# Optimization experiments

Hardware: AMD Instinct MI355X
Metric: run time of the kernel (lower is better)

The kernel has to match this reference:

```python
import jax, jax.numpy as jnp
import numpy as np

N, E, F = 20000, 320000, 128
H = 2 * F  # MLP width = 256
EPS = 1e-5
TANH_ALPHA = 1.0


def setup_inputs() -> dict:
    key = jax.random.key(0)
    ks = jax.random.split(key, 16)
    x = jax.random.normal(ks[0], (N, F), dtype=jnp.float32)
    edge_index = jax.random.randint(ks[1], (2, E), 0, N, dtype=jnp.int64)
    s = 1.0 / np.sqrt(H)
    W1 = jax.random.uniform(ks[2], (H, H), jnp.float32, -s, s)
    b1 = jax.random.uniform(ks[3], (H,), jnp.float32, -s, s)
    g1 = jnp.ones((H,), jnp.float32)
    be1 = jnp.zeros((H,), jnp.float32)
    rm1 = jax.random.normal(ks[4], (H,), jnp.float32) * 0.1
    rv1 = jax.random.uniform(ks[5], (H,), jnp.float32, 0.5, 1.5)
    W2 = jax.random.uniform(ks[6], (H, H), jnp.float32, -s, s)
    b2 = jax.random.uniform(ks[7], (H,), jnp.float32, -s, s)
    g2 = jnp.ones((H,), jnp.float32)
    be2 = jnp.zeros((H,), jnp.float32)
    rm2 = jax.random.normal(ks[8], (H,), jnp.float32) * 0.1
    rv2 = jax.random.uniform(ks[9], (H,), jnp.float32, 0.5, 1.5)
    W3 = jax.random.uniform(ks[10], (F, H), jnp.float32, -s, s)
    b3 = jax.random.uniform(ks[11], (F,), jnp.float32, -s, s)
    return {"x": x, "edge_index": edge_index,
            "W1": W1, "b1": b1, "g1": g1, "be1": be1, "rm1": rm1, "rv1": rv1,
            "W2": W2, "b2": b2, "g2": g2, "be2": be2, "rm2": rm2, "rv2": rv2,
            "W3": W3, "b3": b3}


def _block(h, W, b, g, be, rm, rv):
    # Linear -> (Dropout inactive at eval) -> BatchNorm1d (eval, running stats) -> ReLU
    h = h @ W.T + b
    h = (h - rm) * (g * jax.lax.rsqrt(rv + EPS)) + be
    return jax.nn.relu(h)


def reference(x, edge_index, W1, b1, g1, be1, rm1, rv1,
              W2, b2, g2, be2, rm2, rv2, W3, b3):
    src, dst = edge_index[0], edge_index[1]  # PyG: x_j = x[src], x_i = x[dst]
    xi = x[dst]                              # [E, F]
    xj = x[src]                              # [E, F]
    h = jnp.concatenate([xi, xj - xi], axis=-1)  # [E, 2F]
    h = _block(h, W1, b1, g1, be1, rm1, rv1)
    h = _block(h, W2, b2, g2, be2, rm2, rv2)
    h = h @ W3.T + b3                        # [E, F]
    # scatter-mean aggregation over destination nodes
    summed = jax.ops.segment_sum(h, dst, num_segments=N)              # [N, F]
    cnt = jax.ops.segment_sum(jnp.ones((E,), h.dtype), dst, num_segments=N)
    agg = summed / jnp.maximum(cnt, 1.0)[:, None]
    return jnp.tanh(TANH_ALPHA * agg)
```

## Files before the change

kernel.cpp:

```cpp
#include <hip/hip_runtime.h>
#include <math.h>

#define NN 20000
#define EE 320000
#define FF 128
#define HH 256
#define MT 128

typedef _Float16 f16x8 __attribute__((ext_vector_type(8)));
typedef _Float16 f16x4 __attribute__((ext_vector_type(4)));
typedef float    f32x4 __attribute__((ext_vector_type(4)));

#define HADDR(m, bcol) (((m) << 9) + ((bcol) ^ (((m) & 7) << 4)))

#define WPTR_OFF  80000
#define SPAIR_OFF 160000
#define XH_OFF    1440000
#define W2F_OFF   6560000
#define W3F_OFF   6691072
#define WCF_OFF   6756608
#define PQ_OFF    6887680

#define PB_XH   2500
#define PB_HIST 1250
#define PB_W2   32
#define PB_WC   32
#define PB_W3   16
#define PREP_BLOCKS (PB_XH + PB_HIST + PB_W2 + PB_WC + PB_W3)

#define NODEB 313


__global__ __launch_bounds__(256) void prep_kernel(
    const float* __restrict__ x,  const int* __restrict__ eidx,
    const float* __restrict__ W1, const float* __restrict__ W2,
    const float* __restrict__ W3,
    _Float16* __restrict__ xh, _Float16* __restrict__ w2f,
    _Float16* __restrict__ wcf, _Float16* __restrict__ w3f,
    int* __restrict__ cnt)
{
    const int b = blockIdx.x, t = threadIdx.x;
    if (b < PB_XH) {
        const size_t base = ((size_t)b * 256 + t) * 4;
        float4 v = *(const float4*)(x + base);
        _Float16 o[4] = {(_Float16)v.x, (_Float16)v.y, (_Float16)v.z, (_Float16)v.w};
        __builtin_memcpy(xh + base, o, 8);
    } else if (b < PB_XH + PB_HIST) {
        const int e = (b - PB_XH) * 256 + t;
        atomicAdd(&cnt[eidx[EE + e]], 1);
    } else if (b < PB_XH + PB_HIST + PB_W2) {
        const int f = (b - (PB_XH + PB_HIST)) * 256 + t;
        const int n = ((f >> 9) << 4) | (f & 15);
        const int k = (((f >> 6) & 7) << 5) | (((f >> 4) & 3) << 3);
        const float* s = W2 + (size_t)n * HH + k;
        _Float16 o[8];
        #pragma unroll
        for (int j = 0; j < 8; ++j) o[j] = (_Float16)s[j];
        __builtin_memcpy(w2f + (size_t)f * 8, o, 16);
    } else if (b < PB_XH + PB_HIST + PB_W2 + PB_WC) {
        const int f = (b - (PB_XH + PB_HIST + PB_W2)) * 256 + t;
        const int n = ((f >> 8) << 4) | (f & 15);
        const int k = (((f >> 6) & 3) << 5) | (((f >> 4) & 3) << 3);
        _Float16 o[8];
        if (n < HH) {
            const float* a = W1 + (size_t)n * HH + k;
            #pragma unroll
            for (int j = 0; j < 8; ++j) o[j] = (_Float16)(a[j] - a[FF + j]);
        } else {
            const float* a = W1 + (size_t)(n - HH) * HH + FF + k;
            #pragma unroll
            for (int j = 0; j < 8; ++j) o[j] = (_Float16)a[j];
        }
        __builtin_memcpy(wcf + (size_t)f * 8, o, 16);
    } else {
        const int f = (b - (PB_XH + PB_HIST + PB_W2 + PB_WC)) * 256 + t;
        const int n = ((f >> 9) << 4) | (f & 15);
        const int k = (((f >> 6) & 7) << 5) | (((f >> 4) & 3) << 3);
        const float* s = W3 + (size_t)n * HH + k;
        _Float16 o[8];
        #pragma unroll
        for (int j = 0; j < 8; ++j) o[j] = (_Float16)s[j];
        __builtin_memcpy(w3f + (size_t)f * 8, o, 16);
    }
}

__global__ __launch_bounds__(512) void node_kernel(
    const _Float16* __restrict__ xh, const _Float16* __restrict__ wcf,
    const float* __restrict__ b1, const float* __restrict__ g1,
    const float* __restrict__ be1, const float* __restrict__ rm1,
    const float* __restrict__ rv1,
    _Float16* __restrict__ PQ,
    const int* __restrict__ cnt, int* __restrict__ wptr)
{
    if (blockIdx.x == NODEB) {
        __shared__ int sp[512];
        const int t = threadIdx.x;
        const int base = t * 40;
        int s = 0;
        #pragma unroll 1
        for (int i = 0; i < 40; ++i) { const int idx = base + i; if (idx < NN) s += cnt[idx]; }
        sp[t] = s;
        __syncthreads();
        for (int d = 1; d < 512; d <<= 1) {
            const int v = (t >= d) ? sp[t - d] : 0;
            __syncthreads();
            sp[t] += v;
            __syncthreads();
        }
        int run = sp[t] - s;
        #pragma unroll 1
        for (int i = 0; i < 40; ++i) {
            const int idx = base + i;
            if (idx < NN) { wptr[idx] = run; run += cnt[idx]; }
        }
        return;
    }

    const int tid = threadIdx.x;
    const int lane = tid & 63, wv = tid >> 6;
    const int lr = lane & 15, lq = lane >> 4;
    const int node0 = blockIdx.x * 64;

    f32x4 acc[4][4];
    #pragma unroll
    for (int i = 0; i < 4; ++i)
        #pragma unroll
        for (int j = 0; j < 4; ++j) acc[i][j] = (f32x4){0.f, 0.f, 0.f, 0.f};

    const f16x8* wb = (const f16x8*)wcf + (size_t)(wv * 16) * 64 + lane;
    #pragma unroll 1
    for (int kb = 0; kb < 4; ++kb) {
        f16x8 wf[4], af[4];
        #pragma unroll
        for (int j = 0; j < 4; ++j) wf[j] = wb[(j * 4 + kb) * 64];
        #pragma unroll
        for (int i = 0; i < 4; ++i) {
            int nd = node0 + i * 16 + lr;
            if (nd > NN - 1) nd = NN - 1;
            af[i] = *(const f16x8*)(xh + (size_t)nd * FF + kb * 32 + lq * 8);
        }
        #pragma unroll
        for (int i = 0; i < 4; ++i)
            #pragma unroll
            for (int j = 0; j < 4; ++j)
                acc[i][j] = __builtin_amdgcn_mfma_f32_16x16x32_f16(wf[j], af[i], acc[i][j], 0, 0, 0);
    }

    #pragma unroll
    for (int j = 0; j < 4; ++j) {
        const int n0 = wv * 64 + j * 16 + lq * 4;
        const int ch = (n0 < HH) ? n0 : n0 - HH;
        float sc[4], cc[4];
        #pragma unroll
        for (int r = 0; r < 4; ++r) {
            const float s1 = g1[ch + r] * rsqrtf(rv1[ch + r] + 1e-5f);
            sc[r] = s1;
            cc[r] = (n0 < HH) ? (b1[ch + r] - rm1[ch + r]) * s1 + be1[ch + r] : 0.f;
        }
        #pragma unroll
        for (int i = 0; i < 4; ++i) {
            const int nd = node0 + i * 16 + lr;
            if (nd < NN) {
                f16x4 o;
                #pragma unroll
                for (int r = 0; r < 4; ++r) o[r] = (_Float16)(acc[i][j][r] * sc[r] + cc[r]);
                *(f16x4*)(PQ + (size_t)nd * 512 + n0) = o;
            }
        }
    }
}

__global__ __launch_bounds__(256) void scatter_kernel(const int* __restrict__ eidx,
                                                      int* __restrict__ wptr,
                                                      unsigned int* __restrict__ spair)
{
    const int e = blockIdx.x * 256 + threadIdx.x;
    if (e < EE) {
        const int d = eidx[EE + e];
        const int pos = atomicAdd(&wptr[d], 1);
        spair[pos] = (unsigned int)eidx[e] | ((unsigned int)d << 16);
    }
}

__global__ __launch_bounds__(512, 4) void fused_edge_mlp(
    const _Float16* __restrict__ PQ,
    const unsigned int* __restrict__ spair,
    const _Float16* __restrict__ W2f,
    const float* __restrict__ b2, const float* __restrict__ g2,
    const float* __restrict__ be2, const float* __restrict__ rm2,
    const float* __restrict__ rv2,
    const _Float16* __restrict__ W3f,
    float* __restrict__ outp)
{
    __shared__ __align__(16) char shb[MT * 512];
    __shared__ __align__(16) float s_scale[HH];
    __shared__ __align__(16) float s_c[HH];
    __shared__ int s_dst[MT];

    const int tid = threadIdx.x;
    const int lane = tid & 63, wv = tid >> 6;
    const int lr = lane & 15, lq = lane >> 4;

    const int xcd = blockIdx.x & 7, bi = blockIdx.x >> 3;
    const int swz = (xcd < 4) ? (xcd * 313 + bi) : (1252 + (xcd - 4) * 312 + bi);
    const int e0 = swz * MT;

    {
        const int r = wv * 16 + lr;
        const int q = lq;
        const unsigned int pv = spair[e0 + r];
        const int dr = (int)(pv >> 16), sr = (int)(pv & 0xffffu);
        const f16x8* pd = (const f16x8*)(PQ + (size_t)dr * 512 + q * 64);
        const f16x8* ps = (const f16x8*)(PQ + (size_t)sr * 512 + 256 + q * 64);
        f16x8 av[8], bv[8];
        #pragma unroll
        for (int i = 0; i < 8; ++i) av[i] = pd[i];
        #pragma unroll
        for (int i = 0; i < 8; ++i) bv[i] = ps[i];

        if (tid < MT) s_dst[tid] = (int)(spair[e0 + tid] >> 16);
        if (tid < HH) {
            const float sc = g2[tid] * rsqrtf(rv2[tid] + 1e-5f);
            s_scale[tid] = sc;
            s_c[tid] = (b2[tid] - rm2[tid]) * sc + be2[tid];
        }

        #pragma unroll
        for (int i = 0; i < 8; ++i) {
            f16x8 s = av[i] + bv[i];
            f16x8 o;
            #pragma unroll
            for (int j = 0; j < 8; ++j) {
                const _Float16 z = (_Float16)0;
                o[j] = s[j] > z ? s[j] : z;
            }
            *(f16x8*)(shb + HADDR(r, q * 128 + i * 16)) = o;
        }
    }
    __syncthreads();

    {
        f32x4 acc[8][2];
        #pragma unroll
        for (int i = 0; i < 8; ++i) { acc[i][0] = (f32x4){0.f,0.f,0.f,0.f}; acc[i][1] = (f32x4){0.f,0.f,0.f,0.f}; }

        const int nt0 = wv * 2;
        const f16x8* wbase = (const f16x8*)W2f + lane;
        f16x8 cw0 = wbase[(nt0 * 8) * 64];
        f16x8 cw1 = wbase[((nt0 + 1) * 8) * 64];
        #pragma unroll 1
        for (int kb = 0; kb < 8; ++kb) {
            f16x8 nw0 = wbase[(nt0 * 8 + kb + 1) * 64];
            f16x8 nw1 = wbase[((nt0 + 1) * 8 + kb + 1) * 64];
            #pragma unroll
            for (int h = 0; h < 2; ++h) {
                f16x8 af[4];
                #pragma unroll
                for (int i = 0; i < 4; ++i) {
                    const int m = (h * 4 + i) * 16 + lr;
                    af[i] = *(const f16x8*)(shb + HADDR(m, kb * 64 + lq * 16));
                }
                #pragma unroll
                for (int i = 0; i < 4; ++i) {
                    acc[h*4+i][0] = __builtin_amdgcn_mfma_f32_16x16x32_f16(cw0, af[i], acc[h*4+i][0], 0, 0, 0);
                    acc[h*4+i][1] = __builtin_amdgcn_mfma_f32_16x16x32_f16(cw1, af[i], acc[h*4+i][1], 0, 0, 0);
                }
            }
            cw0 = nw0; cw1 = nw1;
        }
        __syncthreads();
        #pragma unroll
        for (int j = 0; j < 2; ++j) {
            const int n0 = (nt0 + j) * 16 + lq * 4;
            const float4 sc4 = *(const float4*)&s_scale[n0];
            const float4 cc4 = *(const float4*)&s_c[n0];
            #pragma unroll
            for (int i = 0; i < 8; ++i) {
                const int m = i * 16 + lr;
                f16x4 o;
                o[0] = (_Float16)fmaxf(acc[i][j][0] * sc4.x + cc4.x, 0.f);
                o[1] = (_Float16)fmaxf(acc[i][j][1] * sc4.y + cc4.y, 0.f);
                o[2] = (_Float16)fmaxf(acc[i][j][2] * sc4.z + cc4.z, 0.f);
                o[3] = (_Float16)fmaxf(acc[i][j][3] * sc4.w + cc4.w, 0.f);
                *(f16x4*)(shb + HADDR(m, n0 * 2)) = o;
            }
        }
        __syncthreads();
    }

    {
        f32x4 acc[8];
        #pragma unroll
        for (int i = 0; i < 8; ++i) acc[i] = (f32x4){0.f, 0.f, 0.f, 0.f};

        const int nt = wv;
        const f16x8* wbase = (const f16x8*)W3f + lane;
        f16x8 cw = wbase[(nt * 8) * 64];
        #pragma unroll 1
        for (int kb = 0; kb < 8; ++kb) {
            f16x8 nw = wbase[(nt * 8 + kb + 1) * 64];
            #pragma unroll
            for (int h = 0; h < 2; ++h) {
                f16x8 af[4];
                #pragma unroll
                for (int i = 0; i < 4; ++i) {
                    const int m = (h * 4 + i) * 16 + lr;
                    af[i] = *(const f16x8*)(shb + HADDR(m, kb * 64 + lq * 16));
                }
                #pragma unroll
                for (int i = 0; i < 4; ++i)
                    acc[h*4+i] = __builtin_amdgcn_mfma_f32_16x16x32_f16(cw, af[i], acc[h*4+i], 0, 0, 0);
            }
            cw = nw;
        }
        __syncthreads();
        const int n0 = nt * 16 + lq * 4;
        #pragma unroll
        for (int i = 0; i < 8; ++i)
            *(f32x4*)(shb + HADDR(i * 16 + lr, n0 * 4)) = acc[i];
        __syncthreads();

        {
            const int col = tid & 127;
            const int bc = col * 4;
            const int r0 = (tid >> 7) * 32;
            int cur = s_dst[r0];
            float run = 0.f;
            #pragma unroll 1
            for (int r = r0; r < r0 + 32; ++r) {
                const int d = s_dst[r];
                if (d != cur) {
                    atomicAdd(&outp[(size_t)cur * FF + col], run);
                    run = 0.f; cur = d;
                }
                run += *(const float*)(shb + HADDR(r, bc));
            }
            atomicAdd(&outp[(size_t)cur * FF + col], run);
        }
    }
}

__global__ __launch_bounds__(256) void finalize_kernel(const int* __restrict__ cnt,
                                                       const float* __restrict__ b3,
                                                       float* __restrict__ out)
{
    const int i4 = (blockIdx.x * 256 + threadIdx.x) * 4;
    if (i4 < NN * FF) {
        const float c = fmaxf((float)cnt[i4 >> 7], 1.0f);
        const float rc = 1.0f / c;
        float4 v = *(const float4*)(out + i4);
        const float* bb = b3 + (i4 & 127);
        v.x = tanhf(v.x * rc + bb[0]);
        v.y = tanhf(v.y * rc + bb[1]);
        v.z = tanhf(v.z * rc + bb[2]);
        v.w = tanhf(v.w * rc + bb[3]);
        *(float4*)(out + i4) = v;
    }
}

extern "C" void kernel_launch(void* const* d_in, const int* in_sizes, int n_in,
                              void* d_out, int out_size, void* d_ws, size_t ws_size,
                              hipStream_t stream)
{
    const float* x   = (const float*)d_in[0];
    const int*   ei  = (const int*)d_in[1];
    const float* W1  = (const float*)d_in[2];
    const float* b1  = (const float*)d_in[3];
    const float* g1  = (const float*)d_in[4];
    const float* be1 = (const float*)d_in[5];
    const float* rm1 = (const float*)d_in[6];
    const float* rv1 = (const float*)d_in[7];
    const float* W2  = (const float*)d_in[8];
    const float* b2  = (const float*)d_in[9];
    const float* g2  = (const float*)d_in[10];
    const float* be2 = (const float*)d_in[11];
    const float* rm2 = (const float*)d_in[12];
    const float* rv2 = (const float*)d_in[13];
    const float* W3  = (const float*)d_in[14];
    const float* b3  = (const float*)d_in[15];

    char* ws = (char*)d_ws;
    int* cnt_i = (int*)ws;
    int* wptr  = (int*)(ws + WPTR_OFF);
    unsigned int* spair = (unsigned int*)(ws + SPAIR_OFF);
    _Float16* xh  = (_Float16*)(ws + XH_OFF);
    _Float16* w2f = (_Float16*)(ws + W2F_OFF);
    _Float16* w3f = (_Float16*)(ws + W3F_OFF);
    _Float16* wcf = (_Float16*)(ws + WCF_OFF);
    _Float16* PQ  = (_Float16*)(ws + PQ_OFF);
    float* outp = (float*)d_out;

    hipMemsetAsync(cnt_i, 0, NN * sizeof(int), stream);
    hipMemsetAsync(d_out, 0, (size_t)NN * FF * sizeof(float), stream);

    prep_kernel<<<PREP_BLOCKS, 256, 0, stream>>>(x, ei, W1, W2, W3,
                                                 xh, w2f, wcf, w3f, cnt_i);
    node_kernel<<<NODEB + 1, 512, 0, stream>>>(xh, wcf, b1, g1, be1, rm1, rv1,
                                               PQ, cnt_i, wptr);
    scatter_kernel<<<(EE + 255) / 256, 256, 0, stream>>>(ei, wptr, spair);
    fused_edge_mlp<<<EE / MT, 512, 0, stream>>>(PQ, spair,
                                                w2f, b2, g2, be2, rm2, rv2,
                                                w3f, outp);
    finalize_kernel<<<(NN * FF / 4 + 255) / 256, 256, 0, stream>>>(cnt_i, b3, outp);
}
```

Baseline: 278.2 us.

## Fuse all stages into one persistent cooperative kernel with grid syncs

Replaces the memsets and five separate launches with one cooperative kernel of 512 blocks. Stages are separated by grid.sync(): prep, histogram plus node GEMM, prefix scan, scatter, the edge MLP as a persistent tile loop, and finalize. This removes launch gaps and per-kernel ramp-up and tail. In exchange, the scan runs on a single block while the rest of the grid waits at a barrier, and the edge tiles are spread over fewer resident blocks. The segmented-sum loop also batches its shared-memory reads in groups of eight.

```diff
diff --git a/kernel.cpp b/kernel.cpp
--- a/kernel.cpp
+++ b/kernel.cpp
@@ -1,11 +1,15 @@
 #include <hip/hip_runtime.h>
+#include <hip/hip_cooperative_groups.h>
 #include <math.h>
+
+namespace cg = cooperative_groups;
 
 #define NN 20000
 #define EE 320000
 #define FF 128
 #define HH 256
 #define MT 128
+#define NTILE 2500
 
 typedef _Float16 f16x8 __attribute__((ext_vector_type(8)));
 typedef _Float16 f16x4 __attribute__((ext_vector_type(4)));
@@ -21,15 +25,355 @@
 #define WCF_OFF   6756608
 #define PQ_OFF    6887680
 
+#define NODEB 313
+
+
+__global__ __launch_bounds__(512, 4) void mega(
+    const float* x, const int* eidx,
+    const float* W1, const float* b1, const float* g1, const float* be1,
+    const float* rm1, const float* rv1,
+    const float* W2, const float* b2, const float* g2, const float* be2,
+    const float* rm2, const float* rv2,
+    const float* W3, const float* b3,
+    char* ws, float* outp)
+{
+    int* cnt  = (int*)ws;
+    int* wptr = (int*)(ws + WPTR_OFF);
+    unsigned int* spair = (unsigned int*)(ws + SPAIR_OFF);
+    _Float16* xh  = (_Float16*)(ws + XH_OFF);
+    _Float16* w2f = (_Float16*)(ws + W2F_OFF);
+    _Float16* w3f = (_Float16*)(ws + W3F_OFF);
+    _Float16* wcf = (_Float16*)(ws + WCF_OFF);
+    _Float16* PQ  = (_Float16*)(ws + PQ_OFF);
+
+    __shared__ __align__(16) char shb[MT * 512];
+    __shared__ __align__(16) float s_scale[HH];
+    __shared__ __align__(16) float s_c[HH];
+    __shared__ int s_dst[MT];
+
+    cg::grid_group grid = cg::this_grid();
+    const int tid  = threadIdx.x;
+    const int G    = gridDim.x;
+    const int gtid = blockIdx.x * 512 + tid;
+    const int NT   = G * 512;
+    const int lane = tid & 63, wv = tid >> 6;
+    const int lr   = lane & 15, lq = lane >> 4;
+
+    for (int i = gtid; i < 5000; i += NT) ((int4*)cnt)[i] = (int4){0, 0, 0, 0};
+    for (int i = gtid; i < 640000; i += NT) ((float4*)outp)[i] = (float4){0.f, 0.f, 0.f, 0.f};
+    for (int i = gtid; i < 640000; i += NT) {
+        float4 v = ((const float4*)x)[i];
+        _Float16 o[4] = {(_Float16)v.x, (_Float16)v.y, (_Float16)v.z, (_Float16)v.w};
+        __builtin_memcpy(xh + (size_t)i * 4, o, 8);
+    }
+    if (gtid < 8192) {
+        const int f = gtid;
+        const int n = ((f >> 9) << 4) | (f & 15);
+        const int k = (((f >> 6) & 7) << 5) | (((f >> 4) & 3) << 3);
+        const float* s = W2 + (size_t)n * HH + k;
+        _Float16 o[8];
+        #pragma unroll
+        for (int j = 0; j < 8; ++j) o[j] = (_Float16)s[j];
+        __builtin_memcpy(w2f + (size_t)f * 8, o, 16);
+    } else if (gtid < 16384) {
+        const int f = gtid - 8192;
+        const int n = ((f >> 8) << 4) | (f & 15);
+        const int k = (((f >> 6) & 3) << 5) | (((f >> 4) & 3) << 3);
+        _Float16 o[8];
+        if (n < HH) {
+            const float* a = W1 + (size_t)n * HH + k;
+            #pragma unroll
+            for (int j = 0; j < 8; ++j) o[j] = (_Float16)(a[j] - a[FF + j]);
+        } else {
+            const float* a = W1 + (size_t)(n - HH) * HH + FF + k;
+            #pragma unroll
+            for (int j = 0; j < 8; ++j) o[j] = (_Float16)a[j];
+        }
+        __builtin_memcpy(wcf + (size_t)f * 8, o, 16);
+    } else if (gtid < 20480) {
+        const int f = gtid - 16384;
+        const int n = ((f >> 9) << 4) | (f & 15);
+        const int k = (((f >> 6) & 7) << 5) | (((f >> 4) & 3) << 3);
+        const float* s = W3 + (size_t)n * HH + k;
+        _Float16 o[8];
+        #pragma unroll
+        for (int j = 0; j < 8; ++j) o[j] = (_Float16)s[j];
+        __builtin_memcpy(w3f + (size_t)f * 8, o, 16);
+    }
+    grid.sync();
+
+    for (int e = gtid; e < EE; e += NT) atomicAdd(&cnt[eidx[EE + e]], 1);
+
+    if (blockIdx.x < NODEB) {
+        const int node0 = blockIdx.x * 64;
+        f32x4 acc[4][4];
+        #pragma unroll
+        for (int i = 0; i < 4; ++i)
+            #pragma unroll
+            for (int j = 0; j < 4; ++j) acc[i][j] = (f32x4){0.f, 0.f, 0.f, 0.f};
+
+        const f16x8* wb = (const f16x8*)wcf + (size_t)(wv * 16) * 64 + lane;
+        #pragma unroll 1
+        for (int kb = 0; kb < 4; ++kb) {
+            f16x8 wf[4], af[4];
+            #pragma unroll
+            for (int j = 0; j < 4; ++j) wf[j] = wb[(j * 4 + kb) * 64];
+            #pragma unroll
+            for (int i = 0; i < 4; ++i) {
+                int nd = node0 + i * 16 + lr;
+                if (nd > NN - 1) nd = NN - 1;
+                af[i] = *(const f16x8*)(xh + (size_t)nd * FF + kb * 32 + lq * 8);
+            }
+            #pragma unroll
+            for (int i = 0; i < 4; ++i)
+                #pragma unroll
+                for (int j = 0; j < 4; ++j)
+                    acc[i][j] = __builtin_amdgcn_mfma_f32_16x16x32_f16(wf[j], af[i], acc[i][j], 0, 0, 0);
+        }
+        #pragma unroll
+        for (int j = 0; j < 4; ++j) {
+            const int n0 = wv * 64 + j * 16 + lq * 4;
+            const int ch = (n0 < HH) ? n0 : n0 - HH;
+            float sc[4], cc[4];
+            #pragma unroll
+            for (int r = 0; r < 4; ++r) {
+                const float s1 = g1[ch + r] * rsqrtf(rv1[ch + r] + 1e-5f);
+                sc[r] = s1;
+                cc[r] = (n0 < HH) ? (b1[ch + r] - rm1[ch + r]) * s1 + be1[ch + r] : 0.f;
+            }
+            #pragma unroll
+            for (int i = 0; i < 4; ++i) {
+                const int nd = node0 + i * 16 + lr;
+                if (nd < NN) {
+                    f16x4 o;
+                    #pragma unroll
+                    for (int r = 0; r < 4; ++r) o[r] = (_Float16)(acc[i][j][r] * sc[r] + cc[r]);
+                    *(f16x4*)(PQ + (size_t)nd * 512 + n0) = o;
+                }
+            }
+        }
+    }
+    grid.sync();
+
+    if (blockIdx.x == 0) {
+        int* sp = (int*)shb;
+        const int base = tid * 40;
+        int s = 0;
+        #pragma unroll 1
+        for (int g = 0; g < 5; ++g) {
+            int v[8];
+            #pragma unroll
+            for (int u = 0; u < 8; ++u) {
+                const int idx = base + g * 8 + u;
+                v[u] = (idx < NN) ? cnt[idx] : 0;
+            }
+            #pragma unroll
+            for (int u = 0; u < 8; ++u) s += v[u];
+        }
+        sp[tid] = s;
+        __syncthreads();
+        for (int d = 1; d < 512; d <<= 1) {
+            const int v = (tid >= d) ? sp[tid - d] : 0;
+            __syncthreads();
+            sp[tid] += v;
+            __syncthreads();
+        }
+        int run = sp[tid] - s;
+        #pragma unroll 1
+        for (int g = 0; g < 5; ++g) {
+            int v[8];
+            #pragma unroll
+            for (int u = 0; u < 8; ++u) {
+                const int idx = base + g * 8 + u;
+                v[u] = (idx < NN) ? cnt[idx] : 0;
+            }
+            #pragma unroll
+            for (int u = 0; u < 8; ++u) {
+                const int idx = base + g * 8 + u;
+                if (idx < NN) { wptr[idx] = run; run += v[u]; }
+            }
+        }
+    }
+    grid.sync();
+
+    for (int e = gtid; e < EE; e += NT) {
+        const int d = eidx[EE + e];
+        const int pos = atomicAdd(&wptr[d], 1);
+        spair[pos] = (unsigned int)eidx[e] | ((unsigned int)d << 16);
+    }
+    grid.sync();
+
+    if (tid < HH) {
+        const float sc = g2[tid] * rsqrtf(rv2[tid] + 1e-5f);
+        s_scale[tid] = sc;
+        s_c[tid] = (b2[tid] - rm2[tid]) * sc + be2[tid];
+    }
+    #pragma unroll 1
+    for (int tau = blockIdx.x; tau < NTILE; tau += G) {
+        const int xcd = tau & 7, bi = tau >> 3;
+        const int swz = (xcd < 4) ? (xcd * 313 + bi) : (1252 + (xcd - 4) * 312 + bi);
+        const int e0 = swz * MT;
+
+        {
+            const int r = wv * 16 + lr;
+            const int q = lq;
+            const unsigned int pv = spair[e0 + r];
+            const int dr = (int)(pv >> 16), sr = (int)(pv & 0xffffu);
+            const f16x8* pd = (const f16x8*)(PQ + (size_t)dr * 512 + q * 64);
+            const f16x8* ps = (const f16x8*)(PQ + (size_t)sr * 512 + 256 + q * 64);
+            f16x8 av[8], bv[8];
+            #pragma unroll
+            for (int i = 0; i < 8; ++i) av[i] = pd[i];
+            #pragma unroll
+            for (int i = 0; i < 8; ++i) bv[i] = ps[i];
+
+            if (tid < MT) s_dst[tid] = (int)(spair[e0 + tid] >> 16);
+
+            #pragma unroll
+            for (int i = 0; i < 8; ++i) {
+                f16x8 s = av[i] + bv[i];
+                f16x8 o;
+                #pragma unroll
+                for (int j = 0; j < 8; ++j) {
+                    const _Float16 z = (_Float16)0;
+                    o[j] = s[j] > z ? s[j] : z;
+                }
+                *(f16x8*)(shb + HADDR(r, q * 128 + i * 16)) = o;
+            }
+        }
+        __syncthreads();
+
+        {
+            f32x4 acc[8][2];
+            #pragma unroll
+            for (int i = 0; i < 8; ++i) { acc[i][0] = (f32x4){0.f,0.f,0.f,0.f}; acc[i][1] = (f32x4){0.f,0.f,0.f,0.f}; }
+
+            const int nt0 = wv * 2;
+            const f16x8* wbase = (const f16x8*)w2f + lane;
+            f16x8 cw0 = wbase[(nt0 * 8) * 64];
+            f16x8 cw1 = wbase[((nt0 + 1) * 8) * 64];
+            #pragma unroll 1
+            for (int kb = 0; kb < 8; ++kb) {
+                f16x8 nw0 = wbase[(nt0 * 8 + kb + 1) * 64];
+                f16x8 nw1 = wbase[((nt0 + 1) * 8 + kb + 1) * 64];
+                #pragma unroll
+                for (int h = 0; h < 2; ++h) {
+                    f16x8 af[4];
+                    #pragma unroll
+                    for (int i = 0; i < 4; ++i) {
+                        const int m = (h * 4 + i) * 16 + lr;
+                        af[i] = *(const f16x8*)(shb + HADDR(m, kb * 64 + lq * 16));
+                    }
+                    #pragma unroll
+                    for (int i = 0; i < 4; ++i) {
+                        acc[h*4+i][0] = __builtin_amdgcn_mfma_f32_16x16x32_f16(cw0, af[i], acc[h*4+i][0], 0, 0, 0);
+                        acc[h*4+i][1] = __builtin_amdgcn_mfma_f32_16x16x32_f16(cw1, af[i], acc[h*4+i][1], 0, 0, 0);
+                    }
+                }
+                cw0 = nw0; cw1 = nw1;
+            }
+            __syncthreads();
+            #pragma unroll
+            for (int j = 0; j < 2; ++j) {
+                const int n0 = (nt0 + j) * 16 + lq * 4;
+                const float4 sc4 = *(const float4*)&s_scale[n0];
+                const float4 cc4 = *(const float4*)&s_c[n0];
+                #pragma unroll
+                for (int i = 0; i < 8; ++i) {
+                    const int m = i * 16 + lr;
+                    f16x4 o;
+                    o[0] = (_Float16)fmaxf(acc[i][j][0] * sc4.x + cc4.x, 0.f);
+                    o[1] = (_Float16)fmaxf(acc[i][j][1] * sc4.y + cc4.y, 0.f);
+                    o[2] = (_Float16)fmaxf(acc[i][j][2] * sc4.z + cc4.z, 0.f);
+                    o[3] = (_Float16)fmaxf(acc[i][j][3] * sc4.w + cc4.w, 0.f);
+                    *(f16x4*)(shb + HADDR(m, n0 * 2)) = o;
+                }
+            }
+            __syncthreads();
+        }
+
+        {
+            f32x4 acc[8];
+            #pragma unroll
+            for (int i = 0; i < 8; ++i) acc[i] = (f32x4){0.f, 0.f, 0.f, 0.f};
+
+            const int nt = wv;
+            const f16x8* wbase = (const f16x8*)w3f + lane;
+            f16x8 cw = wbase[(nt * 8) * 64];
+            #pragma unroll 1
+            for (int kb = 0; kb < 8; ++kb) {
+                f16x8 nw = wbase[(nt * 8 + kb + 1) * 64];
+                #pragma unroll
+                for (int h = 0; h < 2; ++h) {
+                    f16x8 af[4];
+                    #pragma unroll
+                    for (int i = 0; i < 4; ++i) {
+                        const int m = (h * 4 + i) * 16 + lr;
+                        af[i] = *(const f16x8*)(shb + HADDR(m, kb * 64 + lq * 16));
+                    }
+                    #pragma unroll
+                    for (int i = 0; i < 4; ++i)
+                        acc[h*4+i] = __builtin_amdgcn_mfma_f32_16x16x32_f16(cw, af[i], acc[h*4+i], 0, 0, 0);
+                }
+                cw = nw;
+            }
+            __syncthreads();
+            const int n0 = nt * 16 + lq * 4;
+            #pragma unroll
+            for (int i = 0; i < 8; ++i)
+                *(f32x4*)(shb + HADDR(i * 16 + lr, n0 * 4)) = acc[i];
+            __syncthreads();
+
+            {
+                const int col = tid & 127;
+                const int bc  = col * 4;
+                const int r0  = (tid >> 7) * 32;
+                int cur = s_dst[r0];
+                float run = 0.f;
+                #pragma unroll 1
+                for (int g = 0; g < 4; ++g) {
+                    float v[8];
+                    #pragma unroll
+                    for (int u = 0; u < 8; ++u)
+                        v[u] = *(const float*)(shb + HADDR(r0 + g * 8 + u, bc));
+                    #pragma unroll
+                    for (int u = 0; u < 8; ++u) {
+                        const int r = r0 + g * 8 + u;
+                        const int d = s_dst[r];
+                        if (d != cur) {
+                            atomicAdd(&outp[(size_t)cur * FF + col], run);
+                            run = 0.f; cur = d;
+                        }
+                        run += v[u];
+                    }
+                }
+                atomicAdd(&outp[(size_t)cur * FF + col], run);
+            }
+        }
+        __syncthreads();
+    }
+    grid.sync();
+
+    for (int i = gtid; i < 640000; i += NT) {
+        const int i4 = i * 4;
+        const float c = fmaxf((float)cnt[i4 >> 7], 1.0f);
+        const float rc = 1.0f / c;
+        float4 v = *(const float4*)(outp + i4);
+        const float* bb = b3 + (i4 & 127);
+        v.x = tanhf(v.x * rc + bb[0]);
+        v.y = tanhf(v.y * rc + bb[1]);
+        v.z = tanhf(v.z * rc + bb[2]);
+        v.w = tanhf(v.w * rc + bb[3]);
+        *(float4*)(outp + i4) = v;
+    }
+}
+
 #define PB_XH   2500
 #define PB_HIST 1250
 #define PB_W2   32
 #define PB_WC   32
 #define PB_W3   16
 #define PREP_BLOCKS (PB_XH + PB_HIST + PB_W2 + PB_WC + PB_W3)
-
-#define NODEB 313
-
 
 __global__ __launch_bounds__(256) void prep_kernel(
     const float* __restrict__ x,  const int* __restrict__ eidx,
@@ -115,18 +459,15 @@
         }
         return;
     }
-
     const int tid = threadIdx.x;
     const int lane = tid & 63, wv = tid >> 6;
     const int lr = lane & 15, lq = lane >> 4;
     const int node0 = blockIdx.x * 64;
-
     f32x4 acc[4][4];
     #pragma unroll
     for (int i = 0; i < 4; ++i)
         #pragma unroll
         for (int j = 0; j < 4; ++j) acc[i][j] = (f32x4){0.f, 0.f, 0.f, 0.f};
-
     const f16x8* wb = (const f16x8*)wcf + (size_t)(wv * 16) * 64 + lane;
     #pragma unroll 1
     for (int kb = 0; kb < 4; ++kb) {
@@ -145,7 +486,6 @@
             for (int j = 0; j < 4; ++j)
                 acc[i][j] = __builtin_amdgcn_mfma_f32_16x16x32_f16(wf[j], af[i], acc[i][j], 0, 0, 0);
     }
-
     #pragma unroll
     for (int j = 0; j < 4; ++j) {
         const int n0 = wv * 64 + j * 16 + lq * 4;
@@ -200,7 +540,6 @@
     const int tid = threadIdx.x;
     const int lane = tid & 63, wv = tid >> 6;
     const int lr = lane & 15, lq = lane >> 4;
-
     const int xcd = blockIdx.x & 7, bi = blockIdx.x >> 3;
     const int swz = (xcd < 4) ? (xcd * 313 + bi) : (1252 + (xcd - 4) * 312 + bi);
     const int e0 = swz * MT;
@@ -217,14 +556,12 @@
         for (int i = 0; i < 8; ++i) av[i] = pd[i];
         #pragma unroll
         for (int i = 0; i < 8; ++i) bv[i] = ps[i];
-
         if (tid < MT) s_dst[tid] = (int)(spair[e0 + tid] >> 16);
         if (tid < HH) {
             const float sc = g2[tid] * rsqrtf(rv2[tid] + 1e-5f);
             s_scale[tid] = sc;
             s_c[tid] = (b2[tid] - rm2[tid]) * sc + be2[tid];
         }
-
         #pragma unroll
         for (int i = 0; i < 8; ++i) {
             f16x8 s = av[i] + bv[i];
@@ -243,7 +580,6 @@
         f32x4 acc[8][2];
         #pragma unroll
         for (int i = 0; i < 8; ++i) { acc[i][0] = (f32x4){0.f,0.f,0.f,0.f}; acc[i][1] = (f32x4){0.f,0.f,0.f,0.f}; }
-
         const int nt0 = wv * 2;
         const f16x8* wbase = (const f16x8*)W2f + lane;
         f16x8 cw0 = wbase[(nt0 * 8) * 64];
@@ -292,7 +628,6 @@
         f32x4 acc[8];
         #pragma unroll
         for (int i = 0; i < 8; ++i) acc[i] = (f32x4){0.f, 0.f, 0.f, 0.f};
-
         const int nt = wv;
         const f16x8* wbase = (const f16x8*)W3f + lane;
         f16x8 cw = wbase[(nt * 8) * 64];
@@ -319,7 +654,6 @@
         for (int i = 0; i < 8; ++i)
             *(f32x4*)(shb + HADDR(i * 16 + lr, n0 * 4)) = acc[i];
         __syncthreads();
-
         {
             const int col = tid & 127;
             const int bc = col * 4;
@@ -327,13 +661,21 @@
             int cur = s_dst[r0];
             float run = 0.f;
             #pragma unroll 1
-            for (int r = r0; r < r0 + 32; ++r) {
-                const int d = s_dst[r];
-                if (d != cur) {
-                    atomicAdd(&outp[(size_t)cur * FF + col], run);
-                    run = 0.f; cur = d;
-                }
-                run += *(const float*)(shb + HADDR(r, bc));
+            for (int g = 0; g < 4; ++g) {
+                float v[8];
+                #pragma unroll
+                for (int u = 0; u < 8; ++u)
+                    v[u] = *(const float*)(shb + HADDR(r0 + g * 8 + u, bc));
+                #pragma unroll
+                for (int u = 0; u < 8; ++u) {
+                    const int r = r0 + g * 8 + u;
+                    const int d = s_dst[r];
+                    if (d != cur) {
+                        atomicAdd(&outp[(size_t)cur * FF + col], run);
+                        run = 0.f; cur = d;
+                    }
+                    run += v[u];
+                }
             }
             atomicAdd(&outp[(size_t)cur * FF + col], run);
         }
@@ -380,6 +722,17 @@
     const float* b3  = (const float*)d_in[15];
 
     char* ws = (char*)d_ws;
+    float* outp = (float*)d_out;
+
+    void* kargs[] = { (void*)&x, (void*)&ei, (void*)&W1, (void*)&b1,
+                      (void*)&g1, (void*)&be1, (void*)&rm1, (void*)&rv1,
+                      (void*)&W2, (void*)&b2, (void*)&g2, (void*)&be2,
+                      (void*)&rm2, (void*)&rv2, (void*)&W3, (void*)&b3,
+                      (void*)&ws, (void*)&outp };
+    hipError_t err = hipLaunchCooperativeKernel((const void*)mega, dim3(512), dim3(512),
+                                                kargs, 0, stream);
+    if (err == hipSuccess) return;
+
     int* cnt_i = (int*)ws;
     int* wptr  = (int*)(ws + WPTR_OFF);
     unsigned int* spair = (unsigned int*)(ws + SPAIR_OFF);
@@ -388,18 +741,16 @@
     _Float16* w3f = (_Float16*)(ws + W3F_OFF);
     _Float16* wcf = (_Float16*)(ws + WCF_OFF);
     _Float16* PQ  = (_Float16*)(ws + PQ_OFF);
-    float* outp = (float*)d_out;
 
     hipMemsetAsync(cnt_i, 0, NN * sizeof(int), stream);
     hipMemsetAsync(d_out, 0, (size_t)NN * FF * sizeof(float), stream);
-
     prep_kernel<<<PREP_BLOCKS, 256, 0, stream>>>(x, ei, W1, W2, W3,
                                                  xh, w2f, wcf, w3f, cnt_i);
     node_kernel<<<NODEB + 1, 512, 0, stream>>>(xh, wcf, b1, g1, be1, rm1, rv1,
                                                PQ, cnt_i, wptr);
     scatter_kernel<<<(EE + 255) / 256, 256, 0, stream>>>(ei, wptr, spair);
-    fused_edge_mlp<<<EE / MT, 512, 0, stream>>>(PQ, spair,
-                                                w2f, b2, g2, be2, rm2, rv2,
-                                                w3f, outp);
+    fused_edge_mlp<<<NTILE, 512, 0, stream>>>(PQ, spair,
+                                              w2f, b2, g2, be2, rm2, rv2,
+                                              w3f, outp);
     finalize_kernel<<<(NN * FF / 4 + 255) / 256, 256, 0, stream>>>(cnt_i, b3, outp);
 }
```

Measured after the change: 603.4 us. 2.17x slower.
